# Kernel tuning notes

Measured on AMD Instinct MI355X. Metric: run time of the kernel, lower is better.

The kernel has to match this reference:

```python
import jax, jax.numpy as jnp
import numpy as np

NEG_INF = -2.0**32 + 1.0  # matches torch paddings value


def prelu(x, a):
    return jnp.where(x >= 0, x, a * x)


def setup_inputs() -> dict:
    key = jax.random.key(0)
    ks = jax.random.split(key, 12)
    B, L, D, A = 2048, 200, 128, 64
    return {
        "query": jax.random.normal(ks[0], (B, D), jnp.float32),
        "keys": jax.random.normal(ks[1], (B, L, D), jnp.float32),
        "keys_length": jax.random.randint(ks[2], (B,), 0, L, jnp.int64 if jax.config.jax_enable_x64 else jnp.int32),
        "W1": jax.random.normal(ks[3], (4 * D, A), jnp.float32) * (1.0 / np.sqrt(4 * D)),
        "b1": jax.random.normal(ks[4], (A,), jnp.float32) * 0.01,
        "a1": jnp.full((1,), 0.25, jnp.float32),  # PReLU default init
        "W2": jax.random.normal(ks[5], (A, A), jnp.float32) * (1.0 / np.sqrt(A)),
        "b2": jax.random.normal(ks[6], (A,), jnp.float32) * 0.01,
        "a2": jnp.full((1,), 0.25, jnp.float32),
        "W3": jax.random.normal(ks[7], (A, 1), jnp.float32) * (1.0 / np.sqrt(A)),
        "b3": jax.random.normal(ks[8], (1,), jnp.float32) * 0.01,
    }


def reference(query, keys, keys_length, W1, b1, a1, W2, b2, a2, W3, b3):
    B, L, D = keys.shape
    q = jnp.broadcast_to(query[:, None, :], (B, L, D))
    # concat features: [q, k, q-k, q*k] -> (B, L, 4D)
    q_k = jnp.concatenate([q, keys, q - keys, q * keys], axis=-1)
    h = prelu(jnp.einsum("blf,fa->bla", q_k, W1) + b1, a1)
    h = prelu(jnp.einsum("bla,ac->blc", h, W2) + b2, a2)
    scores = (jnp.einsum("bla,ao->blo", h, W3) + b3)[..., 0]  # (B, L)
    mask = jnp.arange(L)[None, :] < keys_length[:, None]
    scores = jnp.where(mask, scores, NEG_INF)
    att = jax.nn.softmax(scores, axis=1)
    out = jnp.einsum("bl,bld->bd", att, keys)  # bmm(att[:,None,:], keys)
    return out, att
```

## Files before the change

### kernel.cpp

```cpp
#include <hip/hip_runtime.h>
#include <math.h>

typedef __attribute__((ext_vector_type(8))) _Float16 half8;
typedef __attribute__((ext_vector_type(4))) float float4_t;

#define NB 2048
#define LL 200
#define DD 128
#define AA 64
#define NEG_INF_F -4294967295.0f

#define WQ_STRIDE 136

#define WS_WBC_H  0
#define WS_W1D_H  8704
#define WS_W2T_H  17408
#define WS_QA_OFF 43008

__global__ __launch_bounds__(256)
void din_prep(const float* __restrict__ query,
              const float* __restrict__ W1,
              const float* __restrict__ b1,
              const float* __restrict__ W2,
              _Float16* __restrict__ ws16,
              float* __restrict__ qa)
{
    const int tid = threadIdx.x;
    const int blk = blockIdx.x;

    if (blk < 128) {
        __shared__ float sW1s[DD * AA];
        __shared__ float sq[16 * DD];
        const int b0 = blk * 16;
        for (int i = tid; i < DD * AA; i += 256)
            sW1s[i] = W1[i] + W1[2 * DD * AA + i];
        for (int i = tid; i < 16 * DD; i += 256)
            sq[i] = query[(size_t)b0 * DD + i];
        __syncthreads();
        const int lane = tid & 63, bb = tid >> 6;
        for (int g = 0; g < 4; ++g) {
            const int bi = bb * 4 + g;
            float acc = b1[lane];
            #pragma unroll 8
            for (int d = 0; d < DD; ++d)
                acc += sq[bi * DD + d] * sW1s[d * AA + lane];
            qa[(size_t)(b0 + bi) * AA + lane] = acc;
        }
    } else if (blk == 128) {
        for (int i = tid; i < 64 * 17; i += 256) {
            const int a = i / 17, c = i - a * 17;
            half8 hb, hd;
            if (c == 16) {
                #pragma unroll
                for (int j = 0; j < 8; ++j) { hb[j] = (_Float16)0.f; hd[j] = (_Float16)0.f; }
            } else {
                const int d0 = c * 8;
                #pragma unroll
                for (int j = 0; j < 8; ++j) {
                    const int d = d0 + j;
                    hb[j] = (_Float16)(W1[(DD + d) * AA + a] - W1[(2 * DD + d) * AA + a]);
                    hd[j] = (_Float16)(W1[(3 * DD + d) * AA + a]);
                }
            }
            *(half8*)&ws16[WS_WBC_H + a * WQ_STRIDE + c * 8] = hb;
            *(half8*)&ws16[WS_W1D_H + a * WQ_STRIDE + c * 8] = hd;
        }
    } else {
        _Float16* w2t = ws16 + WS_W2T_H;
        const int c = tid >> 2, j0 = (tid & 3) * 16;
        for (int ch = 0; ch < 2; ++ch) {
            half8 v;
            #pragma unroll
            for (int j = 0; j < 8; ++j)
                v[j] = (_Float16)W2[(j0 + ch * 8 + j) * AA + c];
            *(half8*)&w2t[c * AA + j0 + ch * 8] = v;
        }
    }
}

__global__ __launch_bounds__(256, 2)
void din_main(const float* __restrict__ keys,
              const int*   __restrict__ keys_length,
              const float* __restrict__ a1p,
              const float* __restrict__ b2,
              const float* __restrict__ a2p,
              const float* __restrict__ W3,
              const _Float16* __restrict__ ws16,
              const float* __restrict__ qa,
              const float* __restrict__ query,
              float* __restrict__ out,
              float* __restrict__ att)
{
    __shared__ __align__(16) _Float16 sKeys[LL * DD];
    __shared__ __align__(16) _Float16 sWq[AA * WQ_STRIDE];
    __shared__ __align__(16) _Float16 sH1[4 * 16 * 72];
    __shared__ float sQ[136];
    __shared__ float sS[224];
    __shared__ float sRed[16];

    const int tid  = threadIdx.x;
    const int lane = tid & 63, wv = tid >> 6;
    const int col  = lane & 15, quad = lane >> 4;
    const int b    = blockIdx.x;
    const int len  = keys_length[b];
    const float pa1 = a1p[0], pa2 = a2p[0];
    const int Lcap = (len == 0) ? LL : len;

    if (tid < 136) sQ[tid] = (tid < 128) ? query[(size_t)b * DD + tid] : 0.f;
    for (int i = tid; i < 224; i += 256) sS[i] = NEG_INF_F;
    __syncthreads();

    for (int ci = tid; ci < 64 * 17; ci += 256) {
        const int c = ci % 17;
        const int d0 = c * 8;
        const half8 hb = *(const half8*)&ws16[WS_WBC_H + ci * 8];
        const half8 hd = *(const half8*)&ws16[WS_W1D_H + ci * 8];
        half8 r;
        #pragma unroll
        for (int j = 0; j < 8; ++j)
            r[j] = (_Float16)((float)hb[j] + sQ[d0 + j] * (float)hd[j]);
        *(half8*)&sWq[ci * 8] = r;
    }
    for (int i = tid; i < Lcap * 16; i += 256) {
        const int l = i >> 4, c8 = i & 15;
        const float* kp = keys + ((size_t)b * LL + l) * DD + c8 * 8;
        const float4 v0 = *(const float4*)kp;
        const float4 v1 = *(const float4*)(kp + 4);
        half8 h;
        h[0] = (_Float16)v0.x; h[1] = (_Float16)v0.y; h[2] = (_Float16)v0.z; h[3] = (_Float16)v0.w;
        h[4] = (_Float16)v1.x; h[5] = (_Float16)v1.y; h[6] = (_Float16)v1.z; h[7] = (_Float16)v1.w;
        *(half8*)&sKeys[l * DD + ((c8 ^ (l & 7)) << 3)] = h;
    }
    __syncthreads();

    const _Float16* w2t = ws16 + WS_W2T_H;
    half8 w2f[2][4];
    #pragma unroll
    for (int ks = 0; ks < 2; ++ks)
        #pragma unroll
        for (int n = 0; n < 4; ++n)
            w2f[ks][n] = *(const half8*)&w2t[(n * 16 + col) * AA + ks * 32 + quad * 8];
    float qareg[4], b2reg[4], w3reg[4];
    #pragma unroll
    for (int n = 0; n < 4; ++n) {
        qareg[n] = qa[(size_t)b * AA + n * 16 + col];
        b2reg[n] = b2[n * 16 + col];
        w3reg[n] = W3[n * 16 + col];
    }

    const int ntiles = (len + 15) >> 4;
    _Float16* const myH = &sH1[wv * 16 * 72];

    for (int t = wv; t < ntiles; t += 4) {
        const int l0 = t * 16;
        const int lr = (l0 + col < LL) ? (l0 + col) : (LL - 1);

        float4_t C[4] = {{0,0,0,0},{0,0,0,0},{0,0,0,0},{0,0,0,0}};
        #pragma unroll
        for (int ks = 0; ks < 4; ++ks) {
            const int swz = ((ks * 4 + quad) ^ (lr & 7)) << 3;
            const half8 af = *(const half8*)&sKeys[lr * DD + swz];
            const int ko = ks * 32 + quad * 8;
            #pragma unroll
            for (int n = 0; n < 4; ++n) {
                const half8 bf = *(const half8*)&sWq[(n * 16 + col) * WQ_STRIDE + ko];
                C[n] = __builtin_amdgcn_mfma_f32_16x16x32_f16(af, bf, C[n], 0, 0, 0);
            }
        }
        #pragma unroll
        for (int n = 0; n < 4; ++n)
            #pragma unroll
            for (int r = 0; r < 4; ++r) {
                float v = C[n][r] + qareg[n];
                v = v >= 0.f ? v : pa1 * v;
                myH[(quad * 4 + r) * 72 + n * 16 + col] = (_Float16)v;
            }
        float4_t D[4] = {{0,0,0,0},{0,0,0,0},{0,0,0,0},{0,0,0,0}};
        #pragma unroll
        for (int ks = 0; ks < 2; ++ks) {
            const half8 af = *(const half8*)&myH[col * 72 + ks * 32 + quad * 8];
            #pragma unroll
            for (int n = 0; n < 4; ++n)
                D[n] = __builtin_amdgcn_mfma_f32_16x16x32_f16(af, w2f[ks][n], D[n], 0, 0, 0);
        }
        float pr[4] = {0.f, 0.f, 0.f, 0.f};
        #pragma unroll
        for (int n = 0; n < 4; ++n)
            #pragma unroll
            for (int r = 0; r < 4; ++r) {
                float v = D[n][r] + b2reg[n];
                v = v >= 0.f ? v : pa2 * v;
                pr[r] += v * w3reg[n];
            }
        #pragma unroll
        for (int r = 0; r < 4; ++r) {
            float pv = pr[r];
            pv += __shfl_xor(pv, 1);
            pv += __shfl_xor(pv, 2);
            pv += __shfl_xor(pv, 4);
            pv += __shfl_xor(pv, 8);
            const int l = l0 + quad * 4 + r;
            if (col == 0 && l < len) sS[l] = pv;
        }
    }

    __syncthreads();
    float m = (tid < LL) ? sS[tid] : -INFINITY;
    #pragma unroll
    for (int o = 1; o < 64; o <<= 1) m = fmaxf(m, __shfl_xor(m, o));
    if (lane == 0) sRed[wv] = m;
    __syncthreads();
    const float M = fmaxf(fmaxf(sRed[0], sRed[1]), fmaxf(sRed[2], sRed[3]));
    float e = (tid < LL) ? expf(sS[tid] - M) : 0.f;
    float s = e;
    #pragma unroll
    for (int o = 1; o < 64; o <<= 1) s += __shfl_xor(s, o);
    if (lane == 0) sRed[8 + wv] = s;
    __syncthreads();
    const float S = sRed[8] + sRed[9] + sRed[10] + sRed[11];
    const float inv = 1.f / S;
    if (tid < LL) {
        const float v = e * inv;
        sS[tid] = v;
        att[(size_t)b * LL + tid] = v;
    }
    __syncthreads();

    {
        const int c8 = tid & 15, ph = tid >> 4;
        float acc[8];
        #pragma unroll
        for (int j = 0; j < 8; ++j) acc[j] = 0.f;
        for (int l = ph; l < Lcap; l += 16) {
            const float w = sS[l];
            const half8 kv = *(const half8*)&sKeys[l * DD + ((c8 ^ (l & 7)) << 3)];
            #pragma unroll
            for (int j = 0; j < 8; ++j) acc[j] += w * (float)kv[j];
        }
        float* const scratch = (float*)sWq;
        #pragma unroll
        for (int j = 0; j < 8; ++j) scratch[tid * 8 + j] = acc[j];
        __syncthreads();
        if (tid < DD) {
            const int c8o = tid >> 3, j = tid & 7;
            float r = 0.f;
            #pragma unroll
            for (int p = 0; p < 16; ++p) r += scratch[(p * 16 + c8o) * 8 + j];
            out[(size_t)b * DD + tid] = r;
        }
    }
}

extern "C" void kernel_launch(void* const* d_in, const int* in_sizes, int n_in,
                              void* d_out, int out_size, void* d_ws, size_t ws_size,
                              hipStream_t stream) {
    (void)in_sizes; (void)n_in; (void)ws_size; (void)out_size;
    const float* query = (const float*)d_in[0];
    const float* keys  = (const float*)d_in[1];
    const int*   klen  = (const int*)d_in[2];
    const float* W1    = (const float*)d_in[3];
    const float* b1    = (const float*)d_in[4];
    const float* a1    = (const float*)d_in[5];
    const float* W2    = (const float*)d_in[6];
    const float* b2    = (const float*)d_in[7];
    const float* a2    = (const float*)d_in[8];
    const float* W3    = (const float*)d_in[9];

    _Float16* ws16 = (_Float16*)d_ws;
    float*    qawk = (float*)((char*)d_ws + WS_QA_OFF);

    float* out = (float*)d_out;
    float* att = out + (size_t)NB * DD;

    hipLaunchKernelGGL(din_prep, dim3(130), dim3(256), 0, stream,
                       query, W1, b1, W2, ws16, qawk);
    hipLaunchKernelGGL(din_main, dim3(NB), dim3(256), 0, stream,
                       keys, klen, a1, b2, a2, W3, ws16, qawk, query, out, att);
}
```

Baseline: 324.1 us.

## Drop shared-memory key staging and read keys directly from global memory

Removes the 51KB sKeys shared buffer and its staging loop. The MFMA A-fragments and the final weighted sum now load keys straight from global memory as fp32 and convert in registers. The smaller LDS footprint lets launch bounds rise to 4 blocks per CU for more occupancy. Keys are now read twice from global or L2 instead of once, and the output accumulation uses fp32 keys rather than fp16.

```diff
diff --git a/kernel.cpp b/kernel.cpp
--- a/kernel.cpp
+++ b/kernel.cpp
@@ -78,7 +78,7 @@
     }
 }
 
-__global__ __launch_bounds__(256, 2)
+__global__ __launch_bounds__(256, 4)
 void din_main(const float* __restrict__ keys,
               const int*   __restrict__ keys_length,
               const float* __restrict__ a1p,
@@ -91,7 +91,6 @@
               float* __restrict__ out,
               float* __restrict__ att)
 {
-    __shared__ __align__(16) _Float16 sKeys[LL * DD];
     __shared__ __align__(16) _Float16 sWq[AA * WQ_STRIDE];
     __shared__ __align__(16) _Float16 sH1[4 * 16 * 72];
     __shared__ float sQ[136];
@@ -121,17 +120,6 @@
             r[j] = (_Float16)((float)hb[j] + sQ[d0 + j] * (float)hd[j]);
         *(half8*)&sWq[ci * 8] = r;
     }
-    for (int i = tid; i < Lcap * 16; i += 256) {
-        const int l = i >> 4, c8 = i & 15;
-        const float* kp = keys + ((size_t)b * LL + l) * DD + c8 * 8;
-        const float4 v0 = *(const float4*)kp;
-        const float4 v1 = *(const float4*)(kp + 4);
-        half8 h;
-        h[0] = (_Float16)v0.x; h[1] = (_Float16)v0.y; h[2] = (_Float16)v0.z; h[3] = (_Float16)v0.w;
-        h[4] = (_Float16)v1.x; h[5] = (_Float16)v1.y; h[6] = (_Float16)v1.z; h[7] = (_Float16)v1.w;
-        *(half8*)&sKeys[l * DD + ((c8 ^ (l & 7)) << 3)] = h;
-    }
-    __syncthreads();
 
     const _Float16* w2t = ws16 + WS_W2T_H;
     half8 w2f[2][4];
@@ -147,6 +135,7 @@
         b2reg[n] = b2[n * 16 + col];
         w3reg[n] = W3[n * 16 + col];
     }
+    __syncthreads();
 
     const int ntiles = (len + 15) >> 4;
     _Float16* const myH = &sH1[wv * 16 * 72];
@@ -154,13 +143,19 @@
     for (int t = wv; t < ntiles; t += 4) {
         const int l0 = t * 16;
         const int lr = (l0 + col < LL) ? (l0 + col) : (LL - 1);
+        const float* krow = keys + ((size_t)b * LL + lr) * DD;
 
         float4_t C[4] = {{0,0,0,0},{0,0,0,0},{0,0,0,0},{0,0,0,0}};
         #pragma unroll
         for (int ks = 0; ks < 4; ++ks) {
-            const int swz = ((ks * 4 + quad) ^ (lr & 7)) << 3;
-            const half8 af = *(const half8*)&sKeys[lr * DD + swz];
             const int ko = ks * 32 + quad * 8;
+            const float4 v0 = *(const float4*)(krow + ko);
+            const float4 v1 = *(const float4*)(krow + ko + 4);
+            half8 af;
+            af[0] = (_Float16)v0.x; af[1] = (_Float16)v0.y;
+            af[2] = (_Float16)v0.z; af[3] = (_Float16)v0.w;
+            af[4] = (_Float16)v1.x; af[5] = (_Float16)v1.y;
+            af[6] = (_Float16)v1.z; af[7] = (_Float16)v1.w;
             #pragma unroll
             for (int n = 0; n < 4; ++n) {
                 const half8 bf = *(const half8*)&sWq[(n * 16 + col) * WQ_STRIDE + ko];
@@ -228,14 +223,18 @@
 
     {
         const int c8 = tid & 15, ph = tid >> 4;
+        const float* kb = keys + (size_t)b * LL * DD + c8 * 8;
         float acc[8];
         #pragma unroll
         for (int j = 0; j < 8; ++j) acc[j] = 0.f;
         for (int l = ph; l < Lcap; l += 16) {
             const float w = sS[l];
-            const half8 kv = *(const half8*)&sKeys[l * DD + ((c8 ^ (l & 7)) << 3)];
-            #pragma unroll
-            for (int j = 0; j < 8; ++j) acc[j] += w * (float)kv[j];
+            const float4 v0 = *(const float4*)(kb + (size_t)l * DD);
+            const float4 v1 = *(const float4*)(kb + (size_t)l * DD + 4);
+            acc[0] += w * v0.x; acc[1] += w * v0.y;
+            acc[2] += w * v0.z; acc[3] += w * v0.w;
+            acc[4] += w * v1.x; acc[5] += w * v1.y;
+            acc[6] += w * v1.z; acc[7] += w * v1.w;
         }
         float* const scratch = (float*)sWq;
         #pragma unroll
```

Result: slower. 333.8 us (+3.0%).
